# Performance work log

Measured on AMD Instinct MI355X. Metric: run time of the kernel, lower is better.

The kernel has to match this reference:

```python
import jax, jax.numpy as jnp
import numpy as np

EPS = 1e-5  # BatchNorm eps
B, T, D, H, C = 64, 1024, 128, 1024, 128


def _glorot(k, shape):
    lim = float(np.sqrt(6.0 / (shape[0] + shape[1])))
    return jax.random.uniform(k, shape, minval=-lim, maxval=lim, dtype=jnp.float32)


def _bn(x, g, b, m, v):
    # eval-mode BatchNorm1d over the channel (last) dim
    return (x - m) * (g * jax.lax.rsqrt(v + EPS)) + b


def _cell(x, h, c, Wih, Whh, bias):
    # PyTorch LSTM gate order: i, f, g, o
    z = x @ Wih.T + h @ Whh.T + bias
    i, f, g, o = jnp.split(z, 4, axis=-1)
    c = jax.nn.sigmoid(f) * c + jax.nn.sigmoid(i) * jnp.tanh(g)
    h = jax.nn.sigmoid(o) * jnp.tanh(c)
    return h, c


def setup_inputs() -> dict:
    key = jax.random.key(0)
    ks = jax.random.split(key, 24)
    d = {}
    d['x'] = jax.random.normal(ks[0], (B, T, D), dtype=jnp.float32)
    # input BN (eval mode running stats + affine)
    d['ibn_g'] = jnp.ones((D,), jnp.float32); d['ibn_b'] = jnp.zeros((D,), jnp.float32)
    d['ibn_m'] = 0.1 * jax.random.normal(ks[1], (D,), jnp.float32)
    d['ibn_v'] = jnp.ones((D,), jnp.float32)
    # encoder LSTM (2 layers)
    d['enc_Wih0'] = _glorot(ks[2], (4 * H, D)); d['enc_Whh0'] = _glorot(ks[3], (4 * H, H))
    d['enc_b0'] = jnp.zeros((4 * H,), jnp.float32)
    d['enc_Wih1'] = _glorot(ks[4], (4 * H, H)); d['enc_Whh1'] = _glorot(ks[5], (4 * H, H))
    d['enc_b1'] = jnp.zeros((4 * H,), jnp.float32)
    # decoder LSTM (2 layers), layer0 input = num_classes
    d['dec_Wih0'] = _glorot(ks[6], (4 * H, C)); d['dec_Whh0'] = _glorot(ks[7], (4 * H, H))
    d['dec_b0'] = jnp.zeros((4 * H,), jnp.float32)
    d['dec_Wih1'] = _glorot(ks[8], (4 * H, H)); d['dec_Whh1'] = _glorot(ks[9], (4 * H, H))
    d['dec_b1'] = jnp.zeros((4 * H,), jnp.float32)
    # hidden BN
    d['hbn_g'] = jnp.ones((H,), jnp.float32); d['hbn_b'] = jnp.zeros((H,), jnp.float32)
    d['hbn_m'] = 0.1 * jax.random.normal(ks[10], (H,), jnp.float32)
    d['hbn_v'] = jnp.ones((H,), jnp.float32)
    # fc head: Linear(H,H) -> BN -> ReLU -> (Dropout=identity in eval) -> Linear(H,C)
    d['fc1_W'] = _glorot(ks[11], (H, H)); d['fc1_b'] = jnp.zeros((H,), jnp.float32)
    d['fbn_g'] = jnp.ones((H,), jnp.float32); d['fbn_b'] = jnp.zeros((H,), jnp.float32)
    d['fbn_m'] = 0.1 * jax.random.normal(ks[12], (H,), jnp.float32)
    d['fbn_v'] = jnp.ones((H,), jnp.float32)
    d['fc2_W'] = _glorot(ks[13], (C, H)); d['fc2_b'] = jnp.zeros((C,), jnp.float32)
    return d


def reference(x, ibn_g, ibn_b, ibn_m, ibn_v,
              enc_Wih0, enc_Whh0, enc_b0, enc_Wih1, enc_Whh1, enc_b1,
              dec_Wih0, dec_Whh0, dec_b0, dec_Wih1, dec_Whh1, dec_b1,
              hbn_g, hbn_b, hbn_m, hbn_v,
              fc1_W, fc1_b, fbn_g, fbn_b, fbn_m, fbn_v, fc2_W, fc2_b):
    b, t, _ = x.shape
    h = enc_Whh0.shape[1]
    c_dim = fc2_W.shape[0]
    xn = _bn(x, ibn_g, ibn_b, ibn_m, ibn_v)  # (B,T,D), per-channel BN

    def enc_step(carry, xt):
        h0, c0, h1, c1 = carry
        h0, c0 = _cell(xt, h0, c0, enc_Wih0, enc_Whh0, enc_b0)
        h1, c1 = _cell(h0, h1, c1, enc_Wih1, enc_Whh1, enc_b1)
        return (h0, c0, h1, c1), None

    z = jnp.zeros((b, h), x.dtype)
    (h0, c0, h1, c1), _ = jax.lax.scan(enc_step, (z, z, z, z), jnp.swapaxes(xn, 0, 1))

    def dec_step(carry, _):
        d0, e0, d1, e1, y = carry
        d0, e0 = _cell(y, d0, e0, dec_Wih0, dec_Whh0, dec_b0)
        d1, e1 = _cell(d0, d1, e1, dec_Wih1, dec_Whh1, dec_b1)
        hb = _bn(d1, hbn_g, hbn_b, hbn_m, hbn_v)
        f1 = jax.nn.relu(_bn(hb @ fc1_W.T + fc1_b, fbn_g, fbn_b, fbn_m, fbn_v))
        pred = f1 @ fc2_W.T + fc2_b  # (B, C)
        return (d0, e0, d1, e1, pred), pred

    y0 = jnp.zeros((b, c_dim), x.dtype)
    _, preds = jax.lax.scan(dec_step, (h0, c0, h1, c1, y0), None, length=t)
    return jnp.swapaxes(preds, 0, 1)  # (B, T, C)
```

## Files before the change

### kernel.cpp

```cpp
#include <hip/hip_runtime.h>
#include <hip/hip_bf16.h>


typedef __hip_bfloat16 hbf16;
typedef __bf16 bf16x8 __attribute__((ext_vector_type(8)));
typedef float f32x4 __attribute__((ext_vector_type(4)));
#define DEVI static __device__ __forceinline__

#define PITCH 2056
#define PITCH0 1160

DEVI float sigf(float x) { return 1.0f / (1.0f + __expf(-x)); }

DEVI bf16x8 as_bf(f32x4 v) { union { f32x4 f; bf16x8 b; } u; u.f = v; return u.b; }

DEVI void st_u32_coh(void* p, unsigned int v) {
  __hip_atomic_store((unsigned int*)p, v, __ATOMIC_RELAXED, __HIP_MEMORY_SCOPE_AGENT);
}
DEVI void st_u64_coh(void* p, unsigned long long v) {
  __hip_atomic_store((unsigned long long*)p, v, __ATOMIC_RELAXED, __HIP_MEMORY_SCOPE_AGENT);
}
DEVI void st_f32_coh(float* p, float v) {
  __hip_atomic_store(p, v, __ATOMIC_RELAXED, __HIP_MEMORY_SCOPE_AGENT);
}
DEVI unsigned short bf_bits(float v) {
  union { __hip_bfloat16 b; unsigned short s; } u;
  u.b = __float2bfloat16(v);
  return u.s;
}

DEVI void ld32_wait(f32x4* b, const hbf16* ap) {
  asm volatile(
    "global_load_dwordx4 %0, %32, off sc0 sc1\n\t"
    "global_load_dwordx4 %1, %32, off offset:64 sc0 sc1\n\t"
    "global_load_dwordx4 %2, %32, off offset:128 sc0 sc1\n\t"
    "global_load_dwordx4 %3, %32, off offset:192 sc0 sc1\n\t"
    "global_load_dwordx4 %4, %32, off offset:256 sc0 sc1\n\t"
    "global_load_dwordx4 %5, %32, off offset:320 sc0 sc1\n\t"
    "global_load_dwordx4 %6, %32, off offset:384 sc0 sc1\n\t"
    "global_load_dwordx4 %7, %32, off offset:448 sc0 sc1\n\t"
    "global_load_dwordx4 %8, %32, off offset:512 sc0 sc1\n\t"
    "global_load_dwordx4 %9, %32, off offset:576 sc0 sc1\n\t"
    "global_load_dwordx4 %10, %32, off offset:640 sc0 sc1\n\t"
    "global_load_dwordx4 %11, %32, off offset:704 sc0 sc1\n\t"
    "global_load_dwordx4 %12, %32, off offset:768 sc0 sc1\n\t"
    "global_load_dwordx4 %13, %32, off offset:832 sc0 sc1\n\t"
    "global_load_dwordx4 %14, %32, off offset:896 sc0 sc1\n\t"
    "global_load_dwordx4 %15, %32, off offset:960 sc0 sc1\n\t"
    "global_load_dwordx4 %16, %32, off offset:1024 sc0 sc1\n\t"
    "global_load_dwordx4 %17, %32, off offset:1088 sc0 sc1\n\t"
    "global_load_dwordx4 %18, %32, off offset:1152 sc0 sc1\n\t"
    "global_load_dwordx4 %19, %32, off offset:1216 sc0 sc1\n\t"
    "global_load_dwordx4 %20, %32, off offset:1280 sc0 sc1\n\t"
    "global_load_dwordx4 %21, %32, off offset:1344 sc0 sc1\n\t"
    "global_load_dwordx4 %22, %32, off offset:1408 sc0 sc1\n\t"
    "global_load_dwordx4 %23, %32, off offset:1472 sc0 sc1\n\t"
    "global_load_dwordx4 %24, %32, off offset:1536 sc0 sc1\n\t"
    "global_load_dwordx4 %25, %32, off offset:1600 sc0 sc1\n\t"
    "global_load_dwordx4 %26, %32, off offset:1664 sc0 sc1\n\t"
    "global_load_dwordx4 %27, %32, off offset:1728 sc0 sc1\n\t"
    "global_load_dwordx4 %28, %32, off offset:1792 sc0 sc1\n\t"
    "global_load_dwordx4 %29, %32, off offset:1856 sc0 sc1\n\t"
    "global_load_dwordx4 %30, %32, off offset:1920 sc0 sc1\n\t"
    "global_load_dwordx4 %31, %32, off offset:1984 sc0 sc1\n\t"
    "s_waitcnt vmcnt(0)"
    : "=&v"(b[0]), "=&v"(b[1]), "=&v"(b[2]), "=&v"(b[3]),
      "=&v"(b[4]), "=&v"(b[5]), "=&v"(b[6]), "=&v"(b[7]),
      "=&v"(b[8]), "=&v"(b[9]), "=&v"(b[10]), "=&v"(b[11]),
      "=&v"(b[12]), "=&v"(b[13]), "=&v"(b[14]), "=&v"(b[15]),
      "=&v"(b[16]), "=&v"(b[17]), "=&v"(b[18]), "=&v"(b[19]),
      "=&v"(b[20]), "=&v"(b[21]), "=&v"(b[22]), "=&v"(b[23]),
      "=&v"(b[24]), "=&v"(b[25]), "=&v"(b[26]), "=&v"(b[27]),
      "=&v"(b[28]), "=&v"(b[29]), "=&v"(b[30]), "=&v"(b[31])
    : "v"(ap) : "memory");
}

DEVI void ld4x8_wait(f32x4* b, const hbf16* a0, const hbf16* a1,
                     const hbf16* a2, const hbf16* a3) {
  asm volatile(
    "global_load_dwordx4 %0, %32, off sc0 sc1\n\t"
    "global_load_dwordx4 %1, %32, off offset:64 sc0 sc1\n\t"
    "global_load_dwordx4 %2, %32, off offset:128 sc0 sc1\n\t"
    "global_load_dwordx4 %3, %32, off offset:192 sc0 sc1\n\t"
    "global_load_dwordx4 %4, %32, off offset:256 sc0 sc1\n\t"
    "global_load_dwordx4 %5, %32, off offset:320 sc0 sc1\n\t"
    "global_load_dwordx4 %6, %32, off offset:384 sc0 sc1\n\t"
    "global_load_dwordx4 %7, %32, off offset:448 sc0 sc1\n\t"
    "global_load_dwordx4 %8, %33, off sc0 sc1\n\t"
    "global_load_dwordx4 %9, %33, off offset:64 sc0 sc1\n\t"
    "global_load_dwordx4 %10, %33, off offset:128 sc0 sc1\n\t"
    "global_load_dwordx4 %11, %33, off offset:192 sc0 sc1\n\t"
    "global_load_dwordx4 %12, %33, off offset:256 sc0 sc1\n\t"
    "global_load_dwordx4 %13, %33, off offset:320 sc0 sc1\n\t"
    "global_load_dwordx4 %14, %33, off offset:384 sc0 sc1\n\t"
    "global_load_dwordx4 %15, %33, off offset:448 sc0 sc1\n\t"
    "global_load_dwordx4 %16, %34, off sc0 sc1\n\t"
    "global_load_dwordx4 %17, %34, off offset:64 sc0 sc1\n\t"
    "global_load_dwordx4 %18, %34, off offset:128 sc0 sc1\n\t"
    "global_load_dwordx4 %19, %34, off offset:192 sc0 sc1\n\t"
    "global_load_dwordx4 %20, %34, off offset:256 sc0 sc1\n\t"
    "global_load_dwordx4 %21, %34, off offset:320 sc0 sc1\n\t"
    "global_load_dwordx4 %22, %34, off offset:384 sc0 sc1\n\t"
    "global_load_dwordx4 %23, %34, off offset:448 sc0 sc1\n\t"
    "global_load_dwordx4 %24, %35, off sc0 sc1\n\t"
    "global_load_dwordx4 %25, %35, off offset:64 sc0 sc1\n\t"
    "global_load_dwordx4 %26, %35, off offset:128 sc0 sc1\n\t"
    "global_load_dwordx4 %27, %35, off offset:192 sc0 sc1\n\t"
    "global_load_dwordx4 %28, %35, off offset:256 sc0 sc1\n\t"
    "global_load_dwordx4 %29, %35, off offset:320 sc0 sc1\n\t"
    "global_load_dwordx4 %30, %35, off offset:384 sc0 sc1\n\t"
    "global_load_dwordx4 %31, %35, off offset:448 sc0 sc1\n\t"
    "s_waitcnt vmcnt(0)"
    : "=&v"(b[0]), "=&v"(b[1]), "=&v"(b[2]), "=&v"(b[3]),
      "=&v"(b[4]), "=&v"(b[5]), "=&v"(b[6]), "=&v"(b[7]),
      "=&v"(b[8]), "=&v"(b[9]), "=&v"(b[10]), "=&v"(b[11]),
      "=&v"(b[12]), "=&v"(b[13]), "=&v"(b[14]), "=&v"(b[15]),
      "=&v"(b[16]), "=&v"(b[17]), "=&v"(b[18]), "=&v"(b[19]),
      "=&v"(b[20]), "=&v"(b[21]), "=&v"(b[22]), "=&v"(b[23]),
      "=&v"(b[24]), "=&v"(b[25]), "=&v"(b[26]), "=&v"(b[27]),
      "=&v"(b[28]), "=&v"(b[29]), "=&v"(b[30]), "=&v"(b[31])
    : "v"(a0), "v"(a1), "v"(a2), "v"(a3) : "memory");
}

DEVI void gbar(int* cnt8, int e) {
  asm volatile("s_waitcnt vmcnt(0) lgkmcnt(0)" ::: "memory");
  __syncthreads();
  if (threadIdx.x == 0)
    __hip_atomic_fetch_add(&cnt8[(blockIdx.x & 7) * 16], 1,
                           __ATOMIC_RELAXED, __HIP_MEMORY_SCOPE_AGENT);
  if (threadIdx.x < 8) {
    while (__hip_atomic_load(&cnt8[threadIdx.x * 16], __ATOMIC_RELAXED,
                             __HIP_MEMORY_SCOPE_AGENT) < e * 32)
      __builtin_amdgcn_s_sleep(1);
  }
  __syncthreads();
}

DEVI void fill_w(hbf16* W, int pitch, int koff, const hbf16* __restrict__ Wg,
                 int Kg, int base_h) {
  for (int r = (int)(threadIdx.x >> 3); r < 32; r += 32) {
    int g = r >> 3, hc = r & 7;
    const hbf16* src = Wg + (long)(g * 1024 + base_h + hc) * Kg;
    hbf16* dst = W + r * pitch + koff;
    for (int k = (threadIdx.x & 7) * 8; k < Kg; k += 64)
      *reinterpret_cast<bf16x8*>(dst + k) =
          *reinterpret_cast<const bf16x8*>(src + k);
  }
}

DEVI void seg_asm(f32x4& a0, f32x4& a1, const hbf16* __restrict__ A, long lda,
                  const hbf16* W, int pitch, int koff, int w, int q, int r16) {
  const hbf16* ap = A + (long)(w * 16 + r16) * lda + q * 8;
  const hbf16* w0 = W + r16 * pitch + koff + q * 8;
  const hbf16* w1 = W + (16 + r16) * pitch + koff + q * 8;
  f32x4 b[32];
  ld32_wait(b, ap);
#pragma unroll
  for (int k = 0; k < 32; ++k) {
    bf16x8 av = as_bf(b[k]);
    bf16x8 b0 = *reinterpret_cast<const bf16x8*>(w0 + k * 32);
    bf16x8 b1 = *reinterpret_cast<const bf16x8*>(w1 + k * 32);
    a0 = __builtin_amdgcn_mfma_f32_16x16x32_bf16(av, b0, a0, 0, 0, 0);
    a1 = __builtin_amdgcn_mfma_f32_16x16x32_bf16(av, b1, a1, 0, 0, 0);
  }
}

DEVI void seg_x(f32x4& a0, f32x4& a1, const hbf16* __restrict__ A, long lda,
                const hbf16* W, int pitch, int w, int q, int r16) {
  const hbf16* ap = A + (long)(w * 16 + r16) * lda + q * 8;
  const hbf16* w0 = W + r16 * pitch + q * 8;
  const hbf16* w1 = W + (16 + r16) * pitch + q * 8;
#pragma unroll
  for (int k = 0; k < 128; k += 32) {
    bf16x8 av = *reinterpret_cast<const bf16x8*>(ap + k);
    bf16x8 b0 = *reinterpret_cast<const bf16x8*>(w0 + k);
    bf16x8 b1 = *reinterpret_cast<const bf16x8*>(w1 + k);
    a0 = __builtin_amdgcn_mfma_f32_16x16x32_bf16(av, b0, a0, 0, 0, 0);
    a1 = __builtin_amdgcn_mfma_f32_16x16x32_bf16(av, b1, a1, 0, 0, 0);
  }
}

DEVI void mm4_asm(f32x4* pa, const hbf16* __restrict__ abase, const bf16x8* fr) {
  f32x4 b[32];
  ld4x8_wait(b, abase, abase + 16384, abase + 32768, abase + 49152);
#pragma unroll
  for (int i = 0; i < 8; ++i)
#pragma unroll
    for (int mt = 0; mt < 4; ++mt)
      pa[mt] = __builtin_amdgcn_mfma_f32_16x16x32_bf16(
          as_bf(b[mt * 8 + i]), fr[i], pa[mt], 0, 0, 0);
}

DEVI void cell(f32x4 a0, f32x4 a1, float bb0, float bb1, float* cst,
               hbf16* __restrict__ hout, int base_h, int lane, int w) {
  int q = lane >> 4, c = lane & 15;
#pragma unroll
  for (int r = 0; r < 4; ++r) {
    float z0 = a0[r] + bb0;
    float z1 = a1[r] + bb1;
    float zf = __shfl(z0, lane | 8, 64);
    float zo = __shfl(z1, lane | 8, 64);
    float hv = 0.f;
    if (c < 8) {
      float cn = sigf(zf) * cst[r] + sigf(z0) * tanhf(z1);
      cst[r] = cn;
      hv = sigf(zo) * tanhf(cn);
    }
    unsigned short my = bf_bits(hv);
    unsigned short nb = (unsigned short)__shfl((int)my, lane ^ 1, 64);
    if (c < 8 && (c & 1) == 0) {
      unsigned int pk = (unsigned int)my | ((unsigned int)nb << 16);
      st_u32_coh(hout + (long)(w * 16 + q * 4 + r) * 1024 + base_h + c, pk);
    }
  }
}

DEVI void store_c(const float* cst, float* cbuf, int hcol_g, int lane, int w) {
  int q = lane >> 4, c = lane & 15;
  if (c < 8) {
#pragma unroll
    for (int r = 0; r < 4; ++r)
      st_f32_coh(&cbuf[(long)(w * 16 + q * 4 + r) * 1024 + hcol_g], cst[r]);
  }
}

__global__ __launch_bounds__(256, 1) void k_enc(
    const hbf16* __restrict__ xb,
    const hbf16* __restrict__ Wih0f, const hbf16* __restrict__ Whh0,
    const hbf16* __restrict__ Wih1, const hbf16* __restrict__ Whh1,
    const float* __restrict__ b0f, const float* __restrict__ b1f,
    hbf16* h0_0, hbf16* h0_1, hbf16* h1_0, hbf16* h1_1,
    float* c0buf, float* c1buf, int* flags) {
  __shared__ hbf16 W[32 * PITCH];
  int wg = blockIdx.x, tid = threadIdx.x;
  int lane = tid & 63, w = tid >> 6, q = lane >> 4, c = lane & 15;
  bool isL0 = wg < 128;
  int cu = isL0 ? wg : wg - 128;
  int base_h = cu * 8;
  if (isL0) {
    fill_w(W, PITCH0, 0, Wih0f, 128, base_h);
    fill_w(W, PITCH0, 128, Whh0, 1024, base_h);
  } else {
    fill_w(W, PITCH, 0, Wih1, 1024, base_h);
    fill_w(W, PITCH, 1024, Whh1, 1024, base_h);
  }
  __syncthreads();
  const float* bias = isL0 ? b0f : b1f;
  float bb0 = bias[(c >> 3) * 1024 + base_h + (c & 7)];
  float bb1 = bias[(2 + (c >> 3)) * 1024 + base_h + (c & 7)];
  float cst[4] = {0.f, 0.f, 0.f, 0.f};
  int hcol_g = base_h + (c & 7);

  for (int t = 0; t <= 1024; ++t) {
    if (isL0) {
      if (t < 1024) {
        f32x4 a0 = {0.f,0.f,0.f,0.f}, a1 = {0.f,0.f,0.f,0.f};
        const hbf16* h0r = (t & 1) ? h0_0 : h0_1;
        seg_asm(a0, a1, h0r, 1024L, W, PITCH0, 128, w, q, c);
        seg_x(a0, a1, xb + (long)t * 128, 131072L, W, PITCH0, w, q, c);
        hbf16* h0w = (t & 1) ? h0_1 : h0_0;
        cell(a0, a1, bb0, bb1, cst, h0w, base_h, lane, w);
        if (t == 1023) store_c(cst, c0buf, hcol_g, lane, w);
      }
    } else {
      if (t >= 1) {
        f32x4 a0 = {0.f,0.f,0.f,0.f}, a1 = {0.f,0.f,0.f,0.f};
        const hbf16* h0r = (t & 1) ? h0_0 : h0_1;
        seg_asm(a0, a1, h0r, 1024L, W, PITCH, 0, w, q, c);
        const hbf16* h1r = (t & 1) ? h1_1 : h1_0;
        seg_asm(a0, a1, h1r, 1024L, W, PITCH, 1024, w, q, c);
        hbf16* h1w = (t & 1) ? h1_0 : h1_1;
        cell(a0, a1, bb0, bb1, cst, h1w, base_h, lane, w);
        if (t == 1024) store_c(cst, c1buf, hcol_g, lane, w);
      }
    }
    if (t < 1024) gbar(flags, t + 1);
  }
}

__global__ __launch_bounds__(256, 1) void k_dec(
    const hbf16* __restrict__ Wfold, const hbf16* __restrict__ Whh0d,
    const hbf16* __restrict__ Wih1d, const hbf16* __restrict__ Whh1d,
    const float* __restrict__ b0t, const float* __restrict__ b0p,
    const float* __restrict__ b1d,
    const hbf16* __restrict__ fc1Wf, const float* __restrict__ fc1bf,
    const float* __restrict__ fs2, const float* __restrict__ fadd2,
    const hbf16* __restrict__ fc2Wb, const float* __restrict__ fc2b,
    hbf16* d0_0, hbf16* d0_1, hbf16* d1_0, hbf16* d1_1, hbf16* f1b,
    const float* __restrict__ c0buf, const float* __restrict__ c1buf,
    float* __restrict__ out, int* flags) {
  __shared__ hbf16 W[32 * PITCH];
  __shared__ float bounce[4][64][16];
  int wg = blockIdx.x, tid = threadIdx.x;
  int lane = tid & 63, w = tid >> 6, q = lane >> 4, c = lane & 15;
  bool isP1 = wg < 128;
  int cu = isP1 ? wg : wg - 128;
  int base_h = cu * 8;
  if (isP1) {
    fill_w(W, PITCH, 0, Wfold, 1024, base_h);
    fill_w(W, PITCH, 1024, Whh0d, 1024, base_h);
  } else {
    fill_w(W, PITCH, 0, Wih1d, 1024, base_h);
    fill_w(W, PITCH, 1024, Whh1d, 1024, base_h);
  }
  __syncthreads();
  int gi0 = (c >> 3) * 1024 + base_h + (c & 7);
  int gi1 = (2 + (c >> 3)) * 1024 + base_h + (c & 7);
  float bt0, bt1, bp0, bp1;
  if (isP1) { bt0 = b0t[gi0]; bt1 = b0t[gi1]; bp0 = b0p[gi0]; bp1 = b0p[gi1]; }
  else      { bt0 = b1d[gi0]; bt1 = b1d[gi1]; bp0 = bt0;      bp1 = bt1; }
  int hcol_g = base_h + (c & 7);
  float cst[4] = {0.f, 0.f, 0.f, 0.f};
  {
    const float* cb = isP1 ? c0buf : c1buf;
    if (c < 8) {
#pragma unroll
      for (int r = 0; r < 4; ++r)
        cst[r] = cb[(long)(w * 16 + q * 4 + r) * 1024 + hcol_g];
    }
  }
  bool isP3 = (wg < 64);
  bool isPred = (wg >= 128 && wg < 136);
  bf16x8 fr[8];
#pragma unroll
  for (int i = 0; i < 8; ++i) fr[i] = bf16x8{0,0,0,0,0,0,0,0};
  float e_b[4] = {0,0,0,0}, e_s[4] = {0,0,0,0}, e_a[4] = {0,0,0,0};
  int red_row = tid >> 2, red_c4 = (tid & 3) * 4;
  if (isP3) {
    const hbf16* fp = fc1Wf + (long)(wg * 16 + c) * 1024 + w * 256 + q * 8;
#pragma unroll
    for (int i = 0; i < 8; ++i) fr[i] = *reinterpret_cast<const bf16x8*>(fp + i * 32);
#pragma unroll
    for (int i = 0; i < 4; ++i) {
      int col = wg * 16 + red_c4 + i;
      e_b[i] = fc1bf[col]; e_s[i] = fs2[col]; e_a[i] = fadd2[col];
    }
  } else if (isPred) {
    const hbf16* fp = fc2Wb + (long)((wg - 128) * 16 + c) * 1024 + w * 256 + q * 8;
#pragma unroll
    for (int i = 0; i < 8; ++i) fr[i] = *reinterpret_cast<const bf16x8*>(fp + i * 32);
#pragma unroll
    for (int i = 0; i < 4; ++i) e_b[i] = fc2b[(wg - 128) * 16 + red_c4 + i];
  }

  f32x4 r0 = {0.f,0.f,0.f,0.f}, r1 = {0.f,0.f,0.f,0.f};

  for (int t = 0; t <= 1024; ++t) {
    if (isP1 && t < 1024) {
      f32x4 a0 = r0, a1 = r1;
      if (t > 0) {
        seg_asm(a0, a1, f1b, 1024L, W, PITCH, 0, w, q, c);
      } else {
        seg_asm(a0, a1, d0_1, 1024L, W, PITCH, 1024, w, q, c);
      }
      float B0 = (t > 0) ? bt0 : bp0, B1 = (t > 0) ? bt1 : bp1;
      hbf16* d0w = (t & 1) ? d0_1 : d0_0;
      cell(a0, a1, B0, B1, cst, d0w, base_h, lane, w);
    }
    if (!isP1 && t == 0) {
      seg_asm(r0, r1, d1_1, 1024L, W, PITCH, 1024, w, q, c);
    }
    if (isPred && t >= 1) {
      f32x4 pa[4] = {{0.f,0.f,0.f,0.f},{0.f,0.f,0.f,0.f},{0.f,0.f,0.f,0.f},{0.f,0.f,0.f,0.f}};
      mm4_asm(pa, f1b + (long)c * 1024 + w * 256 + q * 8, fr);
#pragma unroll
      for (int mt = 0; mt < 4; ++mt)
#pragma unroll
        for (int r = 0; r < 4; ++r) bounce[w][mt * 16 + q * 4 + r][c] = pa[mt][r];
      __syncthreads();
#pragma unroll
      for (int i = 0; i < 4; ++i) {
        int cc = red_c4 + i;
        float s = bounce[0][red_row][cc] + bounce[1][red_row][cc] +
                  bounce[2][red_row][cc] + bounce[3][red_row][cc] + e_b[i];
        out[(long)red_row * 131072 + (long)(t - 1) * 128 + (wg - 128) * 16 + cc] = s;
      }
    }
    if (t == 1024) break;
    gbar(flags, 3 * t + 1);
    if (!isP1) {
      f32x4 a0 = r0, a1 = r1;
      const hbf16* d0c = (t & 1) ? d0_1 : d0_0;
      seg_asm(a0, a1, d0c, 1024L, W, PITCH, 0, w, q, c);
      hbf16* d1w = (t & 1) ? d1_1 : d1_0;
      cell(a0, a1, bt0, bt1, cst, d1w, base_h, lane, w);
    } else if (isP3 && t < 1023) {
      r0 = f32x4{0.f,0.f,0.f,0.f}; r1 = f32x4{0.f,0.f,0.f,0.f};
      const hbf16* d0n = (t & 1) ? d0_1 : d0_0;
      seg_asm(r0, r1, d0n, 1024L, W, PITCH, 1024, w, q, c);
    }
    gbar(flags, 3 * t + 2);
    if (isP3) {
      const hbf16* d1c = (t & 1) ? d1_1 : d1_0;
      f32x4 pa[4] = {{0.f,0.f,0.f,0.f},{0.f,0.f,0.f,0.f},{0.f,0.f,0.f,0.f},{0.f,0.f,0.f,0.f}};
      mm4_asm(pa, d1c + (long)c * 1024 + w * 256 + q * 8, fr);
#pragma unroll
      for (int mt = 0; mt < 4; ++mt)
#pragma unroll
        for (int r = 0; r < 4; ++r) bounce[w][mt * 16 + q * 4 + r][c] = pa[mt][r];
      __syncthreads();
#pragma unroll
      for (int i = 0; i < 4; ++i) {
        int cc = red_c4 + i;
        float s = bounce[0][red_row][cc] + bounce[1][red_row][cc] +
                  bounce[2][red_row][cc] + bounce[3][red_row][cc];
        float v = fmaxf((s + e_b[i]) * e_s[i] + e_a[i], 0.f);
        bounce[0][red_row][cc] = v;
      }
      {
        union { unsigned short s4[4]; unsigned long long u; } pk;
#pragma unroll
        for (int i = 0; i < 4; ++i) pk.s4[i] = bf_bits(bounce[0][red_row][red_c4 + i]);
        st_u64_coh(f1b + (long)red_row * 1024 + wg * 16 + red_c4, pk.u);
      }
    } else if (isP1 && t < 1023) {
      r0 = f32x4{0.f,0.f,0.f,0.f}; r1 = f32x4{0.f,0.f,0.f,0.f};
      const hbf16* d0n = (t & 1) ? d0_1 : d0_0;
      seg_asm(r0, r1, d0n, 1024L, W, PITCH, 1024, w, q, c);
    }
    if (!isP1 && t < 1023) {
      r0 = f32x4{0.f,0.f,0.f,0.f}; r1 = f32x4{0.f,0.f,0.f,0.f};
      const hbf16* d1n = (t & 1) ? d1_1 : d1_0;
      seg_asm(r0, r1, d1n, 1024L, W, PITCH, 1024, w, q, c);
    }
    gbar(flags, 3 * t + 3);
  }
}


__global__ void k_cast_bf16(const float* __restrict__ s, hbf16* __restrict__ d, long n) {
  long i = (long)blockIdx.x * blockDim.x + threadIdx.x;
  long stride = (long)gridDim.x * blockDim.x;
  for (; i < n; i += stride) d[i] = __float2bfloat16(s[i]);
}

__global__ void k_prep_b0tot(const float* __restrict__ dec_b0, const float* __restrict__ dWih0,
                             const float* __restrict__ fc2b, float* __restrict__ b0d_tot) {
  int n = blockIdx.x * 256 + threadIdx.x;
  float acc = 0.f;
  for (int cc = 0; cc < 128; ++cc) acc += dWih0[n * 128 + cc] * fc2b[cc];
  b0d_tot[n] = dec_b0[n] + acc;
}

__global__ void k_fold_ih0(const float* __restrict__ g, const float* __restrict__ bb,
                           const float* __restrict__ m, const float* __restrict__ v,
                           const float* __restrict__ Wm, const float* __restrict__ b0,
                           hbf16* __restrict__ Wf, float* __restrict__ biasf) {
  int n = blockIdx.x * 256 + threadIdx.x;
  float acc = 0.f;
  for (int k = 0; k < 128; ++k) {
    float s = g[k] * rsqrtf(v[k] + 1e-5f);
    float tt = bb[k] - m[k] * s;
    float wv = Wm[n * 128 + k];
    Wf[n * 128 + k] = __float2bfloat16(wv * s);
    acc += tt * wv;
  }
  biasf[n] = b0[n] + acc;
}

__global__ void k_fold_fc1(const float* __restrict__ hg, const float* __restrict__ hb,
                           const float* __restrict__ hm, const float* __restrict__ hv,
                           const float* __restrict__ Wm, const float* __restrict__ fb,
                           const float* __restrict__ fg, const float* __restrict__ fbb,
                           const float* __restrict__ fm, const float* __restrict__ fv,
                           hbf16* __restrict__ Wf, float* __restrict__ bfo,
                           float* __restrict__ fs2, float* __restrict__ fadd2) {
  int n = blockIdx.x * 256 + threadIdx.x;
  float acc = 0.f;
  for (int k = 0; k < 1024; ++k) {
    float s = hg[k] * rsqrtf(hv[k] + 1e-5f);
    float tt = hb[k] - hm[k] * s;
    float wv = Wm[(long)n * 1024 + k];
    Wf[(long)n * 1024 + k] = __float2bfloat16(wv * s);
    acc += tt * wv;
  }
  bfo[n] = fb[n] + acc;
  float s2 = fg[n] * rsqrtf(fv[n] + 1e-5f);
  fs2[n] = s2;
  fadd2[n] = fbb[n] - fm[n] * s2;
}

__global__ void k_fold_wf(const float* __restrict__ Wih0d, const float* __restrict__ fc2W,
                          hbf16* __restrict__ Wfold) {
  long gid = (long)blockIdx.x * 256 + threadIdx.x;
  int n = (int)(gid >> 10), jcol = (int)(gid & 1023);
  float acc = 0.f;
  for (int cc = 0; cc < 128; ++cc)
    acc += Wih0d[n * 128 + cc] * fc2W[cc * 1024 + jcol];
  Wfold[gid] = __float2bfloat16(acc);
}


extern "C" void kernel_launch(void* const* d_in, const int* in_sizes, int n_in,
                              void* d_out, int out_size, void* d_ws, size_t ws_size,
                              hipStream_t stream) {
  (void)in_sizes; (void)n_in; (void)out_size; (void)ws_size;
  const float* x     = (const float*)d_in[0];
  const float* ibn_g = (const float*)d_in[1];
  const float* ibn_b = (const float*)d_in[2];
  const float* ibn_m = (const float*)d_in[3];
  const float* ibn_v = (const float*)d_in[4];
  const float* eWih0 = (const float*)d_in[5];
  const float* eWhh0 = (const float*)d_in[6];
  const float* e_b0  = (const float*)d_in[7];
  const float* eWih1 = (const float*)d_in[8];
  const float* eWhh1 = (const float*)d_in[9];
  const float* e_b1  = (const float*)d_in[10];
  const float* dWih0 = (const float*)d_in[11];
  const float* dWhh0 = (const float*)d_in[12];
  const float* d_b0  = (const float*)d_in[13];
  const float* dWih1 = (const float*)d_in[14];
  const float* dWhh1 = (const float*)d_in[15];
  const float* d_b1  = (const float*)d_in[16];
  const float* hbn_g = (const float*)d_in[17];
  const float* hbn_b = (const float*)d_in[18];
  const float* hbn_m = (const float*)d_in[19];
  const float* hbn_v = (const float*)d_in[20];
  const float* fc1_W = (const float*)d_in[21];
  const float* fc1_b = (const float*)d_in[22];
  const float* fbn_g = (const float*)d_in[23];
  const float* fbn_b = (const float*)d_in[24];
  const float* fbn_m = (const float*)d_in[25];
  const float* fbn_v = (const float*)d_in[26];
  const float* fc2_W = (const float*)d_in[27];
  const float* fc2_b = (const float*)d_in[28];
  float* out = (float*)d_out;

  char* p = (char*)d_ws;
  auto alloc = [&](size_t bytes) -> void* {
    void* r = (void*)p;
    p += (bytes + 255) & ~(size_t)255;
    return r;
  };
  hbf16* xb     = (hbf16*)alloc(64L * 1024 * 128 * 2);
  hbf16* Wih0f  = (hbf16*)alloc(4096L * 128 * 2);
  hbf16* Whh0e  = (hbf16*)alloc(4096L * 1024 * 2);
  hbf16* Wih1e  = (hbf16*)alloc(4096L * 1024 * 2);
  hbf16* Whh1e  = (hbf16*)alloc(4096L * 1024 * 2);
  hbf16* Wfold  = (hbf16*)alloc(4096L * 1024 * 2);
  hbf16* Whh0d  = (hbf16*)alloc(4096L * 1024 * 2);
  hbf16* Wih1d  = (hbf16*)alloc(4096L * 1024 * 2);
  hbf16* Whh1d  = (hbf16*)alloc(4096L * 1024 * 2);
  hbf16* fc1Wf  = (hbf16*)alloc(1024L * 1024 * 2);
  hbf16* fc2Wb  = (hbf16*)alloc(128L * 1024 * 2);
  float* bias0f = (float*)alloc(4096 * 4);
  float* b0dtot = (float*)alloc(4096 * 4);
  float* fc1bf  = (float*)alloc(1024 * 4);
  float* fs2    = (float*)alloc(1024 * 4);
  float* fadd2  = (float*)alloc(1024 * 4);
  char* st = p;
  hbf16* h0_0 = (hbf16*)alloc(64L * 1024 * 2);
  hbf16* h0_1 = (hbf16*)alloc(64L * 1024 * 2);
  hbf16* h1_0 = (hbf16*)alloc(64L * 1024 * 2);
  hbf16* h1_1 = (hbf16*)alloc(64L * 1024 * 2);
  float* c0b  = (float*)alloc(64L * 1024 * 4);
  float* c1b  = (float*)alloc(64L * 1024 * 4);
  hbf16* f1b  = (hbf16*)alloc(64L * 1024 * 2);
  int*   flagsE = (int*)alloc(256 * 4);
  int*   flagsD = (int*)alloc(256 * 4);
  size_t stbytes = (size_t)(p - st);

  hipMemsetAsync(st, 0, stbytes, stream);

  k_cast_bf16<<<4096, 256, 0, stream>>>(x, xb, 64L * 1024 * 128);
  k_cast_bf16<<<2048, 256, 0, stream>>>(eWhh0, Whh0e, 4096L * 1024);
  k_cast_bf16<<<2048, 256, 0, stream>>>(eWih1, Wih1e, 4096L * 1024);
  k_cast_bf16<<<2048, 256, 0, stream>>>(eWhh1, Whh1e, 4096L * 1024);
  k_cast_bf16<<<2048, 256, 0, stream>>>(dWhh0, Whh0d, 4096L * 1024);
  k_cast_bf16<<<2048, 256, 0, stream>>>(dWih1, Wih1d, 4096L * 1024);
  k_cast_bf16<<<2048, 256, 0, stream>>>(dWhh1, Whh1d, 4096L * 1024);
  k_cast_bf16<<<512, 256, 0, stream>>>(fc2_W, fc2Wb, 128L * 1024);
  k_prep_b0tot<<<16, 256, 0, stream>>>(d_b0, dWih0, fc2_b, b0dtot);
  k_fold_ih0<<<16, 256, 0, stream>>>(ibn_g, ibn_b, ibn_m, ibn_v, eWih0, e_b0, Wih0f, bias0f);
  k_fold_fc1<<<4, 256, 0, stream>>>(hbn_g, hbn_b, hbn_m, hbn_v, fc1_W, fc1_b,
                                    fbn_g, fbn_b, fbn_m, fbn_v, fc1Wf, fc1bf, fs2, fadd2);
  k_fold_wf<<<16384, 256, 0, stream>>>(dWih0, fc2_W, Wfold);

  k_enc<<<256, 256, 0, stream>>>(xb, Wih0f, Whh0e, Wih1e, Whh1e, bias0f, e_b1,
                                 h0_0, h0_1, h1_0, h1_1, c0b, c1b, flagsE);

  k_dec<<<256, 256, 0, stream>>>(Wfold, Whh0d, Wih1d, Whh1d, b0dtot, d_b0, d_b1,
                                 fc1Wf, fc1bf, fs2, fadd2, fc2Wb, fc2_b,
                                 h0_0, h0_1, h1_0, h1_1, f1b, c0b, c1b, out, flagsD);
}
```

Measured before the change: 39.17 ms.

## Reassign decoder recurrent matmuls across workgroups to shorten the critical path per step

Decoder workgroups are regrouped: the layer-0 group now holds Wfold and Whh1d, the layer-1 group holds Wih1d and Whh0d, and the fc1 stage moves to workgroups 192+. Recurrent partial sums (h·Whh) are computed off the critical path by the other group and passed through global partial buffers, which are loaded alongside the activations. The layer-1 group also computes the next d0 recurrent partial in the same pass as its own cell input, sharing the activation loads. The aim is to cut the MFMA work sitting between global barriers on the dependent chain. The cost is extra global stores and loads of fp32 partials each step and larger shared-memory weight tiles.

```diff
diff --git a/kernel.cpp b/kernel.cpp
--- a/kernel.cpp
+++ b/kernel.cpp
@@ -9,6 +9,7 @@
 
 #define PITCH 2056
 #define PITCH0 1160
+#define PITCH1 1032
 
 DEVI float sigf(float x) { return 1.0f / (1.0f + __expf(-x)); }
 
@@ -22,6 +23,10 @@
 }
 DEVI void st_f32_coh(float* p, float v) {
   __hip_atomic_store(p, v, __ATOMIC_RELAXED, __HIP_MEMORY_SCOPE_AGENT);
+}
+DEVI void st16_coh(float* p, f32x4 v) {
+  asm volatile("global_store_dwordx4 %0, %1, off sc0 sc1"
+               :: "v"(p), "v"(v) : "memory");
 }
 DEVI unsigned short bf_bits(float v) {
   union { __hip_bfloat16 b; unsigned short s; } u;
@@ -73,6 +78,56 @@
       "=&v"(b[24]), "=&v"(b[25]), "=&v"(b[26]), "=&v"(b[27]),
       "=&v"(b[28]), "=&v"(b[29]), "=&v"(b[30]), "=&v"(b[31])
     : "v"(ap) : "memory");
+}
+
+DEVI void ld32p2_wait(f32x4* b, f32x4& p0, f32x4& p1, const hbf16* ap,
+                      const float* pp0, const float* pp1) {
+  asm volatile(
+    "global_load_dwordx4 %0, %34, off sc0 sc1\n\t"
+    "global_load_dwordx4 %1, %34, off offset:64 sc0 sc1\n\t"
+    "global_load_dwordx4 %2, %34, off offset:128 sc0 sc1\n\t"
+    "global_load_dwordx4 %3, %34, off offset:192 sc0 sc1\n\t"
+    "global_load_dwordx4 %4, %34, off offset:256 sc0 sc1\n\t"
+    "global_load_dwordx4 %5, %34, off offset:320 sc0 sc1\n\t"
+    "global_load_dwordx4 %6, %34, off offset:384 sc0 sc1\n\t"
+    "global_load_dwordx4 %7, %34, off offset:448 sc0 sc1\n\t"
+    "global_load_dwordx4 %8, %34, off offset:512 sc0 sc1\n\t"
+    "global_load_dwordx4 %9, %34, off offset:576 sc0 sc1\n\t"
+    "global_load_dwordx4 %10, %34, off offset:640 sc0 sc1\n\t"
+    "global_load_dwordx4 %11, %34, off offset:704 sc0 sc1\n\t"
+    "global_load_dwordx4 %12, %34, off offset:768 sc0 sc1\n\t"
+    "global_load_dwordx4 %13, %34, off offset:832 sc0 sc1\n\t"
+    "global_load_dwordx4 %14, %34, off offset:896 sc0 sc1\n\t"
+    "global_load_dwordx4 %15, %34, off offset:960 sc0 sc1\n\t"
+    "global_load_dwordx4 %16, %34, off offset:1024 sc0 sc1\n\t"
+    "global_load_dwordx4 %17, %34, off offset:1088 sc0 sc1\n\t"
+    "global_load_dwordx4 %18, %34, off offset:1152 sc0 sc1\n\t"
+    "global_load_dwordx4 %19, %34, off offset:1216 sc0 sc1\n\t"
+    "global_load_dwordx4 %20, %34, off offset:1280 sc0 sc1\n\t"
+    "global_load_dwordx4 %21, %34, off offset:1344 sc0 sc1\n\t"
+    "global_load_dwordx4 %22, %34, off offset:1408 sc0 sc1\n\t"
+    "global_load_dwordx4 %23, %34, off offset:1472 sc0 sc1\n\t"
+    "global_load_dwordx4 %24, %34, off offset:1536 sc0 sc1\n\t"
+    "global_load_dwordx4 %25, %34, off offset:1600 sc0 sc1\n\t"
+    "global_load_dwordx4 %26, %34, off offset:1664 sc0 sc1\n\t"
+    "global_load_dwordx4 %27, %34, off offset:1728 sc0 sc1\n\t"
+    "global_load_dwordx4 %28, %34, off offset:1792 sc0 sc1\n\t"
+    "global_load_dwordx4 %29, %34, off offset:1856 sc0 sc1\n\t"
+    "global_load_dwordx4 %30, %34, off offset:1920 sc0 sc1\n\t"
+    "global_load_dwordx4 %31, %34, off offset:1984 sc0 sc1\n\t"
+    "global_load_dwordx4 %32, %35, off sc0 sc1\n\t"
+    "global_load_dwordx4 %33, %36, off sc0 sc1\n\t"
+    "s_waitcnt vmcnt(0)"
+    : "=&v"(b[0]), "=&v"(b[1]), "=&v"(b[2]), "=&v"(b[3]),
+      "=&v"(b[4]), "=&v"(b[5]), "=&v"(b[6]), "=&v"(b[7]),
+      "=&v"(b[8]), "=&v"(b[9]), "=&v"(b[10]), "=&v"(b[11]),
+      "=&v"(b[12]), "=&v"(b[13]), "=&v"(b[14]), "=&v"(b[15]),
+      "=&v"(b[16]), "=&v"(b[17]), "=&v"(b[18]), "=&v"(b[19]),
+      "=&v"(b[20]), "=&v"(b[21]), "=&v"(b[22]), "=&v"(b[23]),
+      "=&v"(b[24]), "=&v"(b[25]), "=&v"(b[26]), "=&v"(b[27]),
+      "=&v"(b[28]), "=&v"(b[29]), "=&v"(b[30]), "=&v"(b[31]),
+      "=&v"(p0), "=&v"(p1)
+    : "v"(ap), "v"(pp0), "v"(pp1) : "memory");
 }
 
 DEVI void ld4x8_wait(f32x4* b, const hbf16* a0, const hbf16* a1,
@@ -122,6 +177,20 @@
     : "v"(a0), "v"(a1), "v"(a2), "v"(a3) : "memory");
 }
 
+DEVI void ld2_wait(f32x4& a0, f32x4& a1, const float* pb, int tid) {
+  asm volatile(
+    "global_load_dwordx4 %0, %2, off sc0 sc1\n\t"
+    "global_load_dwordx4 %1, %3, off sc0 sc1\n\t"
+    "s_waitcnt vmcnt(0)"
+    : "=&v"(a0), "=&v"(a1)
+    : "v"(pb + tid * 4), "v"(pb + 1024 + tid * 4) : "memory");
+}
+
+DEVI void dump2(f32x4 a0, f32x4 a1, float* pb, int tid) {
+  st16_coh(pb + tid * 4, a0);
+  st16_coh(pb + 1024 + tid * 4, a1);
+}
+
 DEVI void gbar(int* cnt8, int e) {
   asm volatile("s_waitcnt vmcnt(0) lgkmcnt(0)" ::: "memory");
   __syncthreads();
@@ -162,6 +231,49 @@
     bf16x8 b1 = *reinterpret_cast<const bf16x8*>(w1 + k * 32);
     a0 = __builtin_amdgcn_mfma_f32_16x16x32_bf16(av, b0, a0, 0, 0, 0);
     a1 = __builtin_amdgcn_mfma_f32_16x16x32_bf16(av, b1, a1, 0, 0, 0);
+  }
+}
+
+DEVI void seg_cin(f32x4& a0, f32x4& a1, const hbf16* __restrict__ A,
+                  const float* pb, int tid, const hbf16* W,
+                  int w, int q, int r16) {
+  const hbf16* ap = A + (long)(w * 16 + r16) * 1024L + q * 8;
+  const hbf16* w0 = W + r16 * PITCH1 + q * 8;
+  const hbf16* w1 = W + (16 + r16) * PITCH1 + q * 8;
+  f32x4 b[32];
+  ld32p2_wait(b, a0, a1, ap, pb + tid * 4, pb + 1024 + tid * 4);
+#pragma unroll
+  for (int k = 0; k < 32; ++k) {
+    bf16x8 av = as_bf(b[k]);
+    bf16x8 b0 = *reinterpret_cast<const bf16x8*>(w0 + k * 32);
+    bf16x8 b1 = *reinterpret_cast<const bf16x8*>(w1 + k * 32);
+    a0 = __builtin_amdgcn_mfma_f32_16x16x32_bf16(av, b0, a0, 0, 0, 0);
+    a1 = __builtin_amdgcn_mfma_f32_16x16x32_bf16(av, b1, a1, 0, 0, 0);
+  }
+}
+
+DEVI void seg2_cin(f32x4& a0, f32x4& a1, f32x4& r0, f32x4& r1,
+                   const hbf16* __restrict__ A, const float* pb, int tid,
+                   const hbf16* W, int w, int q, int r16) {
+  const hbf16* ap = A + (long)(w * 16 + r16) * 1024L + q * 8;
+  const hbf16* w0 = W + r16 * PITCH1 + q * 8;
+  const hbf16* w1 = W + (16 + r16) * PITCH1 + q * 8;
+  const hbf16* w2 = W + (32 + r16) * PITCH1 + q * 8;
+  const hbf16* w3 = W + (48 + r16) * PITCH1 + q * 8;
+  f32x4 b[32];
+  ld32p2_wait(b, a0, a1, ap, pb + tid * 4, pb + 1024 + tid * 4);
+  r0 = f32x4{0.f,0.f,0.f,0.f}; r1 = f32x4{0.f,0.f,0.f,0.f};
+#pragma unroll
+  for (int k = 0; k < 32; ++k) {
+    bf16x8 av = as_bf(b[k]);
+    a0 = __builtin_amdgcn_mfma_f32_16x16x32_bf16(
+        av, *reinterpret_cast<const bf16x8*>(w0 + k * 32), a0, 0, 0, 0);
+    a1 = __builtin_amdgcn_mfma_f32_16x16x32_bf16(
+        av, *reinterpret_cast<const bf16x8*>(w1 + k * 32), a1, 0, 0, 0);
+    r0 = __builtin_amdgcn_mfma_f32_16x16x32_bf16(
+        av, *reinterpret_cast<const bf16x8*>(w2 + k * 32), r0, 0, 0, 0);
+    r1 = __builtin_amdgcn_mfma_f32_16x16x32_bf16(
+        av, *reinterpret_cast<const bf16x8*>(w3 + k * 32), r1, 0, 0, 0);
   }
 }
 
@@ -288,51 +400,52 @@
     const hbf16* __restrict__ fc2Wb, const float* __restrict__ fc2b,
     hbf16* d0_0, hbf16* d0_1, hbf16* d1_0, hbf16* d1_1, hbf16* f1b,
     const float* __restrict__ c0buf, const float* __restrict__ c1buf,
+    float* pbuf0, float* pbuf1,
     float* __restrict__ out, int* flags) {
-  __shared__ hbf16 W[32 * PITCH];
+  __shared__ hbf16 W[64 * PITCH1];
   __shared__ float bounce[4][64][16];
   int wg = blockIdx.x, tid = threadIdx.x;
   int lane = tid & 63, w = tid >> 6, q = lane >> 4, c = lane & 15;
-  bool isP1 = wg < 128;
-  int cu = isP1 ? wg : wg - 128;
-  int base_h = cu * 8;
-  if (isP1) {
-    fill_w(W, PITCH, 0, Wfold, 1024, base_h);
-    fill_w(W, PITCH, 1024, Whh0d, 1024, base_h);
+  bool isRY = wg < 128;
+  int n = isRY ? wg : wg - 128;
+  int base_h = n * 8;
+  if (isRY) {
+    fill_w(W, PITCH1, 0, Wfold, 1024, base_h);
+    fill_w(W + 32 * PITCH1, PITCH1, 0, Whh1d, 1024, base_h);
   } else {
-    fill_w(W, PITCH, 0, Wih1d, 1024, base_h);
-    fill_w(W, PITCH, 1024, Whh1d, 1024, base_h);
+    fill_w(W, PITCH1, 0, Wih1d, 1024, base_h);
+    fill_w(W + 32 * PITCH1, PITCH1, 0, Whh0d, 1024, base_h);
   }
   __syncthreads();
   int gi0 = (c >> 3) * 1024 + base_h + (c & 7);
   int gi1 = (2 + (c >> 3)) * 1024 + base_h + (c & 7);
   float bt0, bt1, bp0, bp1;
-  if (isP1) { bt0 = b0t[gi0]; bt1 = b0t[gi1]; bp0 = b0p[gi0]; bp1 = b0p[gi1]; }
+  if (isRY) { bt0 = b0t[gi0]; bt1 = b0t[gi1]; bp0 = b0p[gi0]; bp1 = b0p[gi1]; }
   else      { bt0 = b1d[gi0]; bt1 = b1d[gi1]; bp0 = bt0;      bp1 = bt1; }
   int hcol_g = base_h + (c & 7);
   float cst[4] = {0.f, 0.f, 0.f, 0.f};
   {
-    const float* cb = isP1 ? c0buf : c1buf;
+    const float* cb = isRY ? c0buf : c1buf;
     if (c < 8) {
 #pragma unroll
       for (int r = 0; r < 4; ++r)
         cst[r] = cb[(long)(w * 16 + q * 4 + r) * 1024 + hcol_g];
     }
   }
-  bool isP3 = (wg < 64);
   bool isPred = (wg >= 128 && wg < 136);
+  bool isF1 = (wg >= 192);
   bf16x8 fr[8];
 #pragma unroll
   for (int i = 0; i < 8; ++i) fr[i] = bf16x8{0,0,0,0,0,0,0,0};
   float e_b[4] = {0,0,0,0}, e_s[4] = {0,0,0,0}, e_a[4] = {0,0,0,0};
   int red_row = tid >> 2, red_c4 = (tid & 3) * 4;
-  if (isP3) {
-    const hbf16* fp = fc1Wf + (long)(wg * 16 + c) * 1024 + w * 256 + q * 8;
+  if (isF1) {
+    const hbf16* fp = fc1Wf + (long)((wg - 192) * 16 + c) * 1024 + w * 256 + q * 8;
 #pragma unroll
     for (int i = 0; i < 8; ++i) fr[i] = *reinterpret_cast<const bf16x8*>(fp + i * 32);
 #pragma unroll
     for (int i = 0; i < 4; ++i) {
-      int col = wg * 16 + red_c4 + i;
+      int col = (wg - 192) * 16 + red_c4 + i;
       e_b[i] = fc1bf[col]; e_s[i] = fs2[col]; e_a[i] = fadd2[col];
     }
   } else if (isPred) {
@@ -343,22 +456,28 @@
     for (int i = 0; i < 4; ++i) e_b[i] = fc2b[(wg - 128) * 16 + red_c4 + i];
   }
 
-  f32x4 r0 = {0.f,0.f,0.f,0.f}, r1 = {0.f,0.f,0.f,0.f};
+  if (!isRY) {
+    f32x4 r0 = {0.f,0.f,0.f,0.f}, r1 = {0.f,0.f,0.f,0.f};
+    seg_asm(r0, r1, d0_1, 1024L, W + 32 * PITCH1, PITCH1, 0, w, q, c);
+    dump2(r0, r1, pbuf0 + n * 2048, tid);
+  } else {
+    f32x4 r0 = {0.f,0.f,0.f,0.f}, r1 = {0.f,0.f,0.f,0.f};
+    seg_asm(r0, r1, d1_1, 1024L, W + 32 * PITCH1, PITCH1, 0, w, q, c);
+    dump2(r0, r1, pbuf1 + n * 2048, tid);
+  }
+  gbar(flags, 1);
 
   for (int t = 0; t <= 1024; ++t) {
-    if (isP1 && t < 1024) {
-      f32x4 a0 = r0, a1 = r1;
+    if (isRY && t < 1024) {
+      f32x4 a0, a1;
       if (t > 0) {
-        seg_asm(a0, a1, f1b, 1024L, W, PITCH, 0, w, q, c);
+        seg_cin(a0, a1, f1b, pbuf0 + n * 2048, tid, W, w, q, c);
       } else {
-        seg_asm(a0, a1, d0_1, 1024L, W, PITCH, 1024, w, q, c);
+        ld2_wait(a0, a1, pbuf0 + n * 2048, tid);
       }
       float B0 = (t > 0) ? bt0 : bp0, B1 = (t > 0) ? bt1 : bp1;
       hbf16* d0w = (t & 1) ? d0_1 : d0_0;
       cell(a0, a1, B0, B1, cst, d0w, base_h, lane, w);
-    }
-    if (!isP1 && t == 0) {
-      seg_asm(r0, r1, d1_1, 1024L, W, PITCH, 1024, w, q, c);
     }
     if (isPred && t >= 1) {
       f32x4 pa[4] = {{0.f,0.f,0.f,0.f},{0.f,0.f,0.f,0.f},{0.f,0.f,0.f,0.f},{0.f,0.f,0.f,0.f}};
@@ -377,20 +496,23 @@
       }
     }
     if (t == 1024) break;
-    gbar(flags, 3 * t + 1);
-    if (!isP1) {
-      f32x4 a0 = r0, a1 = r1;
+    gbar(flags, 3 * t + 2);
+    if (!isRY) {
+      f32x4 a0, a1, r0, r1;
       const hbf16* d0c = (t & 1) ? d0_1 : d0_0;
-      seg_asm(a0, a1, d0c, 1024L, W, PITCH, 0, w, q, c);
+      seg2_cin(a0, a1, r0, r1, d0c, pbuf1 + n * 2048, tid, W, w, q, c);
       hbf16* d1w = (t & 1) ? d1_1 : d1_0;
       cell(a0, a1, bt0, bt1, cst, d1w, base_h, lane, w);
-    } else if (isP3 && t < 1023) {
-      r0 = f32x4{0.f,0.f,0.f,0.f}; r1 = f32x4{0.f,0.f,0.f,0.f};
-      const hbf16* d0n = (t & 1) ? d0_1 : d0_0;
-      seg_asm(r0, r1, d0n, 1024L, W, PITCH, 1024, w, q, c);
-    }
-    gbar(flags, 3 * t + 2);
-    if (isP3) {
+      if (t < 1023) dump2(r0, r1, pbuf0 + n * 2048, tid);
+    }
+    gbar(flags, 3 * t + 3);
+    if (isRY && t < 1023) {
+      f32x4 r0 = {0.f,0.f,0.f,0.f}, r1 = {0.f,0.f,0.f,0.f};
+      const hbf16* d1c = (t & 1) ? d1_1 : d1_0;
+      seg_asm(r0, r1, d1c, 1024L, W + 32 * PITCH1, PITCH1, 0, w, q, c);
+      dump2(r0, r1, pbuf1 + n * 2048, tid);
+    }
+    if (isF1) {
       const hbf16* d1c = (t & 1) ? d1_1 : d1_0;
       f32x4 pa[4] = {{0.f,0.f,0.f,0.f},{0.f,0.f,0.f,0.f},{0.f,0.f,0.f,0.f},{0.f,0.f,0.f,0.f}};
       mm4_asm(pa, d1c + (long)c * 1024 + w * 256 + q * 8, fr);
@@ -411,19 +533,10 @@
         union { unsigned short s4[4]; unsigned long long u; } pk;
 #pragma unroll
         for (int i = 0; i < 4; ++i) pk.s4[i] = bf_bits(bounce[0][red_row][red_c4 + i]);
-        st_u64_coh(f1b + (long)red_row * 1024 + wg * 16 + red_c4, pk.u);
+        st_u64_coh(f1b + (long)red_row * 1024 + (wg - 192) * 16 + red_c4, pk.u);
       }
-    } else if (isP1 && t < 1023) {
-      r0 = f32x4{0.f,0.f,0.f,0.f}; r1 = f32x4{0.f,0.f,0.f,0.f};
-      const hbf16* d0n = (t & 1) ? d0_1 : d0_0;
-      seg_asm(r0, r1, d0n, 1024L, W, PITCH, 1024, w, q, c);
-    }
-    if (!isP1 && t < 1023) {
-      r0 = f32x4{0.f,0.f,0.f,0.f}; r1 = f32x4{0.f,0.f,0.f,0.f};
-      const hbf16* d1n = (t & 1) ? d1_1 : d1_0;
-      seg_asm(r0, r1, d1n, 1024L, W, PITCH, 1024, w, q, c);
-    }
-    gbar(flags, 3 * t + 3);
+    }
+    gbar(flags, 3 * t + 4);
   }
 }
 
@@ -548,6 +661,8 @@
   float* fc1bf  = (float*)alloc(1024 * 4);
   float* fs2    = (float*)alloc(1024 * 4);
   float* fadd2  = (float*)alloc(1024 * 4);
+  float* pbuf0  = (float*)alloc(128L * 2048 * 4);
+  float* pbuf1  = (float*)alloc(128L * 2048 * 4);
   char* st = p;
   hbf16* h0_0 = (hbf16*)alloc(64L * 1024 * 2);
   hbf16* h0_1 = (hbf16*)alloc(64L * 1024 * 2);
@@ -581,5 +696,6 @@
 
   k_dec<<<256, 256, 0, stream>>>(Wfold, Whh0d, Wih1d, Whh1d, b0dtot, d_b0, d_b1,
                                  fc1Wf, fc1bf, fs2, fadd2, fc2Wb, fc2_b,
-                                 h0_0, h0_1, h1_0, h1_1, f1b, c0b, c1b, out, flagsD);
-}
+                                 h0_0, h0_1, h1_0, h1_1, f1b, c0b, c1b,
+                                 pbuf0, pbuf1, out, flagsD);
+}
```

Result: slower. 45.24 ms (+15.5%).
